# Kernel optimization log

Hardware: AMD Instinct MI355X
Metric: run time of the kernel (lower is better)

The kernel has to match this reference:

```python
import jax, jax.numpy as jnp
import numpy as np

B, T, F, N = 262144, 3, 17, 8
EMBD = 32
DT = 0.2  # 25/5*0.04
EPS = 1e-8  # torch.cosine_similarity eps


def _mono(x, wi, bi, wo, bo):
    # monotonic_fun with increasing=False: relu(-Linear(x)) -> Linear
    h = jax.nn.relu(-(x @ wi.T + bi))  # (..., EMBD)
    return h @ wo.T + bo               # (..., 1)


def _cos(a, b):
    dot = jnp.sum(a * b, axis=-1)
    na = jnp.maximum(jnp.linalg.norm(a, axis=-1), EPS)
    nb = jnp.maximum(jnp.linalg.norm(b, axis=-1), EPS)
    return dot / (na * nb)


def _angle_clamp(vec, e, ang):
    # vec: (B,K,2), e: (B,2) -> keep forces within effective angle cone, sum over K
    keep = jnp.abs(_cos(e[:, None, :], vec)) > ang
    return jnp.sum(vec * keep[..., None], axis=1)


def setup_inputs() -> dict:
    key = jax.random.key(0)
    ks = jax.random.split(key, 8)
    ego = jax.random.normal(ks[0], (B, T, F), jnp.float32)
    ego = ego.at[:, :, 2:4].multiply(10.0)  # position scale
    nei = jax.random.normal(ks[1], (B, N, F), jnp.float32)
    nei = nei.at[:, :, 2:4].multiply(10.0).at[:, :, 4:6].multiply(0.1)
    border = jax.random.normal(ks[2], (4,), jnp.float32)
    attr_dest_para = jax.random.uniform(ks[3], (2,), jnp.float32) + 0.1  # relu(rand), keep away from 0 divisor
    eff_angle = jax.nn.sigmoid(jax.random.uniform(ks[4], (1,), jnp.float32))

    def mlp(k):
        k1, k2, k3, k4 = jax.random.split(k, 4)
        wi = jax.random.uniform(k1, (EMBD, 1), jnp.float32)      # clamped >= 0
        bi = jax.random.normal(k2, (EMBD,), jnp.float32) * 0.1
        wo = jax.random.uniform(k3, (1, EMBD), jnp.float32) * 0.1  # clamped >= 0
        bo = jax.random.normal(k4, (1,), jnp.float32) * 0.1
        return wi, bi, wo, bo

    an = mlp(ks[5])
    rn = mlp(ks[6])
    rb = mlp(ks[7])
    dl = mlp(jax.random.fold_in(key, 99))
    return dict(
        ego=ego, nei=nei, border=border,
        attr_dest_para=attr_dest_para, eff_angle=eff_angle,
        an_wi=an[0], an_bi=an[1], an_wo=an[2], an_bo=an[3],
        rn_wi=rn[0], rn_bi=rn[1], rn_wo=rn[2], rn_bo=rn[3],
        rb_wi=rb[0], rb_bi=rb[1], rb_wo=rb[2], rb_bo=rb[3],
        dl_wi=dl[0], dl_bi=dl[1], dl_wo=dl[2], dl_bo=dl[3],
    )


def reference(ego, nei, border, attr_dest_para, eff_angle,
              an_wi, an_bi, an_wo, an_bo,
              rn_wi, rn_bi, rn_wo, rn_bo,
              rb_wi, rb_bi, rb_wo, rb_bo,
              dl_wi, dl_bi, dl_wo, dl_bo):
    ego_last = ego[:, -1]  # (B,F)

    # --- attr_destination (desired_velocity=None branch) ---
    v34 = ego_last[:, 3:5]
    dv = jnp.stack([jnp.linalg.norm(v34, axis=-1),
                    jnp.zeros(ego.shape[0], ego.dtype)], axis=1)  # (B,2)
    f_dest = ((attr_dest_para[1] * dv - v34) / attr_dest_para[0])[:, None, :]  # (B,1,2)

    # --- attr_repu_neighbors ---
    r = nei[:, :, 2:4] - ego_last[:, None, 2:4]  # (B,N,2)
    mask = nei[:, :, 2:4] == 0                    # (B,N,2)
    r_norm = jnp.linalg.norm(r, axis=-1, keepdims=True)  # (B,N,1)

    # neighbor durality: quirky use of batch element 1, shared across batch
    ids_last = ego[1, -1, 8:-1]  # (8,) neighbor-id columns
    dur = jnp.zeros(N, ego.dtype)
    for t in range(ego.shape[1]):
        dur = dur + jnp.isin(ids_last, ego[1, t, 8:-1]).astype(ego.dtype)

    f_attr = _mono(r_norm, an_wi, an_bi, an_wo, an_bo) * r / r_norm \
             * _mono(dur[:, None], dl_wi, dl_bi, dl_wo, dl_bo)  # (B,N,2)*(N,1)
    f_attr = jnp.where(mask, 0.0, f_attr)

    v_nei = nei[:, :, 4:6]
    b = r_norm \
        + jnp.sum((r + v_nei * DT) ** 2, axis=-1, keepdims=True) \
        - jnp.sum((v_nei * DT) ** 2, axis=-1, keepdims=True)
    b = jnp.sqrt(b) / 2
    f_repu = _mono(b, rn_wi, rn_bi, rn_wo, rn_bo) * r / r_norm
    f_repu = jnp.where(mask, 0.0, f_repu)

    # --- repu_borders (select_lane = [0, -1]) ---
    rb_all = ego_last[:, 3, None] - border        # (B,4)
    rbv = jnp.stack([rb_all[:, 0], rb_all[:, -1]], axis=1)  # (B,2)
    rbn = jnp.abs(rbv)
    f_bor = _mono(rbn[..., None], rb_wi, rb_bi, rb_wo, rb_bo) * (rbv / rbn)[..., None]  # (B,2,1)
    f_bor = jnp.concatenate([jnp.zeros_like(f_bor), f_bor], axis=-1)  # (B,2,2): [0, fy]

    # --- angle clamp + integrate ---
    e = ego_last[:, 4:6]
    e = e / jnp.linalg.norm(e, axis=1, keepdims=True)
    a = (_angle_clamp(f_dest, e, eff_angle)
         + _angle_clamp(f_attr, e, eff_angle) + _angle_clamp(f_repu, e, eff_angle)
         + _angle_clamp(f_bor, e, eff_angle))
    v = ego_last[:, 2:4] + a * DT
    s = ego_last[:, :2] + v * DT
    return jnp.concatenate([s, v, a], axis=1)  # (B,6)
```

## Files before the change

kernel.cpp:

```cpp
#include <hip/hip_runtime.h>

#define DTC 0.2f
#define EPSC 1e-8f


__global__ __launch_bounds__(128) void sfm_pre(
    const float* __restrict__ ego,
    const float* __restrict__ an_wi, const float* __restrict__ an_bi, const float* __restrict__ an_wo,
    const float* __restrict__ rn_wi, const float* __restrict__ rn_bi, const float* __restrict__ rn_wo,
    const float* __restrict__ rb_wi, const float* __restrict__ rb_bi, const float* __restrict__ rb_wo,
    const float* __restrict__ dl_wi, const float* __restrict__ dl_bi,
    const float* __restrict__ dl_wo, const float* __restrict__ dl_bo,
    float* __restrict__ ws)
{
    __shared__ float tk[96], wiwo[96], wobi[96], skn[96], ssw[96], ssb[96];
    int t = threadIdx.x;
    if (t < 96) {
        int f = t >> 5, k = t & 31;
        const float* wip = (f == 0) ? an_wi : ((f == 1) ? rn_wi : rb_wi);
        const float* bip = (f == 0) ? an_bi : ((f == 1) ? rn_bi : rb_bi);
        const float* wop = (f == 0) ? an_wo : ((f == 1) ? rn_wo : rb_wo);
        float wi = wip[k], bi = bip[k], wo = wop[k];
        tk[t]   = -bi / wi;
        wiwo[t] = wi * wo;
        wobi[t] = wo * bi;
    }
    __syncthreads();
    if (t < 96) {
        int f = t >> 5, k = t & 31;
        float my = tk[t];
        int rank = 0;
        for (int m = 0; m < 32; ++m) {
            float o = tk[f * 32 + m];
            rank += (o < my || (o == my && m < k)) ? 1 : 0;
        }
        skn[f * 32 + rank] = my;
        ssw[f * 32 + rank] = wiwo[t];
        ssb[f * 32 + rank] = wobi[t];
    }
    __syncthreads();
    if (t < 96) {
        int f = t >> 5, p = t & 31;
        float sw_ = 0.f, sb_ = 0.f;
        for (int m = p; m < 32; ++m) { sw_ += ssw[f * 32 + m]; sb_ += ssb[f * 32 + m]; }
        int base = 16 + f * 112;
        ws[base + p]      = skn[f * 32 + p];
        ws[base + 32 + p] = sw_;
        ws[base + 65 + p] = sb_;
        if (p == 0) { ws[base + 64] = 0.f; ws[base + 97] = 0.f; }
    }
    if (t >= 96 && t < 104) {
        int j = t - 96;
        const float* base = ego + 51;
        float idv = base[2 * 17 + 8 + j];
        float dur = 0.f;
        for (int tt = 0; tt < 3; ++tt) {
            bool fo = false;
            for (int m = 0; m < 8; ++m) fo = fo || (idv == base[tt * 17 + 8 + m]);
            dur += fo ? 1.f : 0.f;
        }
        float acc = 0.f;
        for (int k = 0; k < 32; ++k)
            acc = fmaf(dl_wo[k], fmaxf(0.f, -fmaf(dl_wi[k], dur, dl_bi[k])), acc);
        ws[j] = acc + dl_bo[0];
    }
}

__device__ __forceinline__ float mono_eval(const float* __restrict__ kn, float x) {
    int i = (kn[15] <= x) ? 16 : 0;
    i += (kn[i + 7] <= x) ? 8 : 0;
    i += (kn[i + 3] <= x) ? 4 : 0;
    i += (kn[i + 1] <= x) ? 2 : 0;
    i += (kn[i] <= x) ? 1 : 0;
    return -fmaf(kn[32 + i], x, kn[65 + i]);
}

__global__ __launch_bounds__(256) void sfm_main(
    const float* __restrict__ ego, const float* __restrict__ nei,
    const float* __restrict__ border, const float* __restrict__ adp,
    const float* __restrict__ eang,
    const float* __restrict__ an_bo, const float* __restrict__ rn_bo,
    const float* __restrict__ rb_bo,
    const float* __restrict__ wsrc,
    float* __restrict__ out, int Bn)
{
    __shared__ float sw[360];
    __shared__ float snei[4352];
    __shared__ float sego[1632];
    __shared__ float sout[192];

    int t = threadIdx.x;
    long long blk = blockIdx.x;

    {
        const float4* nsrc = (const float4*)nei + blk * 1088;
        long long ntot = (long long)Bn * 34;
        float4* nd = (float4*)snei;
#pragma unroll
        for (int i = 0; i < 5; ++i) {
            int idx = t + 256 * i;
            if (idx < 1088 && blk * 1088 + idx < ntot) nd[idx] = nsrc[idx];
        }
        const float4* esrc = (const float4*)ego + blk * 408;
        long long etot = (long long)Bn * 51 / 4;
        float4* ed = (float4*)sego;
#pragma unroll
        for (int i = 0; i < 2; ++i) {
            int idx = t + 256 * i;
            if (idx < 408 && blk * 408 + idx < etot) ed[idx] = esrc[idx];
        }
    }
    for (int i = t; i < 352; i += 256) sw[i] = wsrc[i];
    if (t == 0) sw[352] = an_bo[0];
    if (t == 1) sw[353] = rn_bo[0];
    if (t == 2) sw[354] = rb_bo[0];
    if (t == 3) sw[355] = adp[0];
    if (t == 4) sw[356] = adp[1];
    if (t == 5) sw[357] = eang[0];
    if (t == 6) sw[358] = border[0];
    if (t == 7) sw[359] = border[3];
    __syncthreads();

    int l  = t & 7;
    int r32 = t >> 3;

    const float* eg = sego + 51 * r32 + 34;
    float g0 = eg[0], g1 = eg[1], g2 = eg[2], g3 = eg[3], g4 = eg[4], g5 = eg[5];

    const float* nr = snei + 136 * r32 + 17 * l + 2;
    float nx = nr[0], ny = nr[1], vx = nr[2], vy = nr[3];

    float Rx = nx - g2, Ry = ny - g3;
    float rr = sqrtf(Rx * Rx + Ry * Ry);
    float ax = fmaf(vx, DTC, Rx), ay = fmaf(vy, DTC, Ry);
    float wx = vx * DTC, wy = vy * DTC;
    float bb = sqrtf(rr + ax * ax + ay * ay - wx * wx - wy * wy) * 0.5f;

    float an_bo_v = sw[352], rn_bo_v = sw[353], rb_bo_v = sw[354];
    float p0 = sw[355], p1 = sw[356], ang = sw[357];
    float rb0 = g3 - sw[358], rb1 = g3 - sw[359];
    float rbn0 = fabsf(rb0), rbn1 = fabsf(rb1);

    float fA = mono_eval(sw + 16, rr) + an_bo_v;
    float fR = mono_eval(sw + 128, bb) + rn_bo_v;
    float xb = (l == 1) ? rbn1 : rbn0;
    float vB = 0.f;
    if (l < 2) vB = mono_eval(sw + 240, xb) + rb_bo_v;
    int lb = (t & 63) & ~7;
    float vB0 = __shfl(vB, lb + 0, 64);
    float vB1 = __shfl(vB, lb + 1, 64);

    float elen = sqrtf(g4 * g4 + g5 * g5);
    float ex = g4 / elen, ey = g5 / elen;
    float na = fmaxf(sqrtf(ex * ex + ey * ey), EPSC);

    float axs = 0.f, ays = 0.f;
#define CLAMP_ADD(VX, VY)                                                   \
    {                                                                       \
        float _vx = (VX), _vy = (VY);                                       \
        float _nv = fmaxf(sqrtf(_vx * _vx + _vy * _vy), EPSC);              \
        float _c = (ex * _vx + ey * _vy) / (na * _nv);                      \
        if (fabsf(_c) > ang) { axs += _vx; ays += _vy; }                    \
    }

    float mfx = (nx == 0.f) ? 0.f : 1.f;
    float mfy = (ny == 0.f) ? 0.f : 1.f;

    {
        float coef = fA / rr * sw[l];
        CLAMP_ADD(coef * Rx * mfx, coef * Ry * mfy);
    }
    {
        float coef = fR / rr;
        CLAMP_ADD(coef * Rx * mfx, coef * Ry * mfy);
    }

#pragma unroll
    for (int m = 1; m < 8; m <<= 1) {
        axs += __shfl_xor(axs, m, 64);
        ays += __shfl_xor(ays, m, 64);
    }

    if (l == 0) {
        float dvn = sqrtf(g3 * g3 + g4 * g4);
        CLAMP_ADD((p1 * dvn - g3) / p0, -g4 / p0);
        CLAMP_ADD(0.f, vB0 * (rb0 / rbn0));
        CLAMP_ADD(0.f, vB1 * (rb1 / rbn1));

        float vxo = fmaf(axs, DTC, g2);
        float vyo = fmaf(ays, DTC, g3);
        float* op = sout + 6 * r32;
        op[0] = fmaf(vxo, DTC, g0);
        op[1] = fmaf(vyo, DTC, g1);
        op[2] = vxo; op[3] = vyo;
        op[4] = axs; op[5] = ays;
    }
#undef CLAMP_ADD

    __syncthreads();
    if (t < 192) {
        long long o = blk * 192 + t;
        if (o < (long long)Bn * 6) out[o] = sout[t];
    }
}

extern "C" void kernel_launch(void* const* d_in, const int* in_sizes, int n_in,
                              void* d_out, int out_size, void* d_ws, size_t ws_size,
                              hipStream_t stream) {
    const float* ego    = (const float*)d_in[0];
    const float* nei    = (const float*)d_in[1];
    const float* border = (const float*)d_in[2];
    const float* adp    = (const float*)d_in[3];
    const float* eang   = (const float*)d_in[4];
    const float* an_wi  = (const float*)d_in[5];
    const float* an_bi  = (const float*)d_in[6];
    const float* an_wo  = (const float*)d_in[7];
    const float* an_bo  = (const float*)d_in[8];
    const float* rn_wi  = (const float*)d_in[9];
    const float* rn_bi  = (const float*)d_in[10];
    const float* rn_wo  = (const float*)d_in[11];
    const float* rn_bo  = (const float*)d_in[12];
    const float* rb_wi  = (const float*)d_in[13];
    const float* rb_bi  = (const float*)d_in[14];
    const float* rb_wo  = (const float*)d_in[15];
    const float* rb_bo  = (const float*)d_in[16];
    const float* dl_wi  = (const float*)d_in[17];
    const float* dl_bi  = (const float*)d_in[18];
    const float* dl_wo  = (const float*)d_in[19];
    const float* dl_bo  = (const float*)d_in[20];
    float* out = (float*)d_out;
    float* ws  = (float*)d_ws;

    int Bn = in_sizes[0] / (3 * 17);

    sfm_pre<<<1, 128, 0, stream>>>(ego,
                                   an_wi, an_bi, an_wo,
                                   rn_wi, rn_bi, rn_wo,
                                   rb_wi, rb_bi, rb_wo,
                                   dl_wi, dl_bi, dl_wo, dl_bo, ws);

    int grid = (Bn + 31) / 32;
    sfm_main<<<grid, 256, 0, stream>>>(ego, nei, border, adp, eang,
                                       an_bo, rn_bo, rb_bo,
                                       ws, out, Bn);
}
```

Before: 289.7 us.

## Fuse preprocessing into persistent grid-stride main kernel

Merges the single-block weight-preprocessing kernel into the main kernel, so every block recomputes the sorted knot tables into shared memory and no second launch or workspace round trip is needed. The main kernel becomes persistent: a fixed grid of 1536 blocks loops over 32-row tiles. The output store is also widened to float4. In exchange, each block repeats the small preprocessing work, and each tile iteration now has extra barriers with no overlap between loading and compute.

```diff
diff --git a/kernel.cpp b/kernel.cpp
--- a/kernel.cpp
+++ b/kernel.cpp
@@ -4,50 +4,69 @@
 #define EPSC 1e-8f
 
 
-__global__ __launch_bounds__(128) void sfm_pre(
-    const float* __restrict__ ego,
-    const float* __restrict__ an_wi, const float* __restrict__ an_bi, const float* __restrict__ an_wo,
-    const float* __restrict__ rn_wi, const float* __restrict__ rn_bi, const float* __restrict__ rn_wo,
-    const float* __restrict__ rb_wi, const float* __restrict__ rb_bi, const float* __restrict__ rb_wo,
+__device__ __forceinline__ float mono_eval(const float* __restrict__ kn, float x) {
+    int i = (kn[15] <= x) ? 16 : 0;
+    i += (kn[i + 7] <= x) ? 8 : 0;
+    i += (kn[i + 3] <= x) ? 4 : 0;
+    i += (kn[i + 1] <= x) ? 2 : 0;
+    i += (kn[i] <= x) ? 1 : 0;
+    return -fmaf(kn[32 + i], x, kn[65 + i]);
+}
+
+__global__ __launch_bounds__(256, 6) void sfm_fused(
+    const float* __restrict__ ego, const float* __restrict__ nei,
+    const float* __restrict__ border, const float* __restrict__ adp,
+    const float* __restrict__ eang,
+    const float* __restrict__ an_wi, const float* __restrict__ an_bi,
+    const float* __restrict__ an_wo, const float* __restrict__ an_bo,
+    const float* __restrict__ rn_wi, const float* __restrict__ rn_bi,
+    const float* __restrict__ rn_wo, const float* __restrict__ rn_bo,
+    const float* __restrict__ rb_wi, const float* __restrict__ rb_bi,
+    const float* __restrict__ rb_wo, const float* __restrict__ rb_bo,
     const float* __restrict__ dl_wi, const float* __restrict__ dl_bi,
     const float* __restrict__ dl_wo, const float* __restrict__ dl_bo,
-    float* __restrict__ ws)
+    float* __restrict__ out, int Bn)
 {
-    __shared__ float tk[96], wiwo[96], wobi[96], skn[96], ssw[96], ssb[96];
+    __shared__ __align__(16) float sw[360];
+    __shared__ __align__(16) float snei[4352];
+    __shared__ __align__(16) float sego[1632];
+    __shared__ __align__(16) float sout[192];
+
     int t = threadIdx.x;
+
     if (t < 96) {
         int f = t >> 5, k = t & 31;
         const float* wip = (f == 0) ? an_wi : ((f == 1) ? rn_wi : rb_wi);
         const float* bip = (f == 0) ? an_bi : ((f == 1) ? rn_bi : rb_bi);
         const float* wop = (f == 0) ? an_wo : ((f == 1) ? rn_wo : rb_wo);
         float wi = wip[k], bi = bip[k], wo = wop[k];
-        tk[t]   = -bi / wi;
-        wiwo[t] = wi * wo;
-        wobi[t] = wo * bi;
+        snei[t]       = -bi / wi;
+        snei[96 + t]  = wi * wo;
+        snei[192 + t] = wo * bi;
     }
     __syncthreads();
     if (t < 96) {
         int f = t >> 5, k = t & 31;
-        float my = tk[t];
+        float my = snei[t];
         int rank = 0;
         for (int m = 0; m < 32; ++m) {
-            float o = tk[f * 32 + m];
+            float o = snei[f * 32 + m];
             rank += (o < my || (o == my && m < k)) ? 1 : 0;
         }
-        skn[f * 32 + rank] = my;
-        ssw[f * 32 + rank] = wiwo[t];
-        ssb[f * 32 + rank] = wobi[t];
+        snei[288 + f * 32 + rank] = my;
+        snei[384 + f * 32 + rank] = snei[96 + t];
+        snei[480 + f * 32 + rank] = snei[192 + t];
     }
     __syncthreads();
     if (t < 96) {
         int f = t >> 5, p = t & 31;
         float sw_ = 0.f, sb_ = 0.f;
-        for (int m = p; m < 32; ++m) { sw_ += ssw[f * 32 + m]; sb_ += ssb[f * 32 + m]; }
+        for (int m = p; m < 32; ++m) { sw_ += snei[384 + f * 32 + m]; sb_ += snei[480 + f * 32 + m]; }
         int base = 16 + f * 112;
-        ws[base + p]      = skn[f * 32 + p];
-        ws[base + 32 + p] = sw_;
-        ws[base + 65 + p] = sb_;
-        if (p == 0) { ws[base + 64] = 0.f; ws[base + 97] = 0.f; }
+        sw[base + p]      = snei[288 + f * 32 + p];
+        sw[base + 32 + p] = sw_;
+        sw[base + 65 + p] = sb_;
+        if (p == 0) { sw[base + 64] = 0.f; sw[base + 97] = 0.f; }
     }
     if (t >= 96 && t < 104) {
         int j = t - 96;
@@ -62,145 +81,117 @@
         float acc = 0.f;
         for (int k = 0; k < 32; ++k)
             acc = fmaf(dl_wo[k], fmaxf(0.f, -fmaf(dl_wi[k], dur, dl_bi[k])), acc);
-        ws[j] = acc + dl_bo[0];
-    }
-}
-
-__device__ __forceinline__ float mono_eval(const float* __restrict__ kn, float x) {
-    int i = (kn[15] <= x) ? 16 : 0;
-    i += (kn[i + 7] <= x) ? 8 : 0;
-    i += (kn[i + 3] <= x) ? 4 : 0;
-    i += (kn[i + 1] <= x) ? 2 : 0;
-    i += (kn[i] <= x) ? 1 : 0;
-    return -fmaf(kn[32 + i], x, kn[65 + i]);
-}
-
-__global__ __launch_bounds__(256) void sfm_main(
-    const float* __restrict__ ego, const float* __restrict__ nei,
-    const float* __restrict__ border, const float* __restrict__ adp,
-    const float* __restrict__ eang,
-    const float* __restrict__ an_bo, const float* __restrict__ rn_bo,
-    const float* __restrict__ rb_bo,
-    const float* __restrict__ wsrc,
-    float* __restrict__ out, int Bn)
-{
-    __shared__ float sw[360];
-    __shared__ float snei[4352];
-    __shared__ float sego[1632];
-    __shared__ float sout[192];
-
-    int t = threadIdx.x;
-    long long blk = blockIdx.x;
-
-    {
-        const float4* nsrc = (const float4*)nei + blk * 1088;
-        long long ntot = (long long)Bn * 34;
-        float4* nd = (float4*)snei;
+        sw[j] = acc + dl_bo[0];
+    }
+    if (t == 104) sw[352] = an_bo[0];
+    if (t == 105) sw[353] = rn_bo[0];
+    if (t == 106) sw[354] = rb_bo[0];
+    if (t == 107) sw[355] = adp[0];
+    if (t == 108) sw[356] = adp[1];
+    if (t == 109) sw[357] = eang[0];
+    if (t == 110) sw[358] = border[0];
+    if (t == 111) sw[359] = border[3];
+    __syncthreads();
+
+    int l   = t & 7;
+    int r32 = t >> 3;
+    long long nTiles = ((long long)Bn + 31) >> 5;
+
+    for (long long tt = blockIdx.x; tt < nTiles; tt += gridDim.x) {
+        {
+            const float4* nsrc = (const float4*)nei + tt * 1088;
+            float4* nd = (float4*)snei;
 #pragma unroll
-        for (int i = 0; i < 5; ++i) {
-            int idx = t + 256 * i;
-            if (idx < 1088 && blk * 1088 + idx < ntot) nd[idx] = nsrc[idx];
-        }
-        const float4* esrc = (const float4*)ego + blk * 408;
-        long long etot = (long long)Bn * 51 / 4;
-        float4* ed = (float4*)sego;
+            for (int i = 0; i < 5; ++i) {
+                int idx = t + 256 * i;
+                if (idx < 1088 && tt * 1088 + idx < (long long)Bn * 34) nd[idx] = nsrc[idx];
+            }
+            const float4* esrc = (const float4*)ego + tt * 408;
+            float4* ed = (float4*)sego;
 #pragma unroll
-        for (int i = 0; i < 2; ++i) {
-            int idx = t + 256 * i;
-            if (idx < 408 && blk * 408 + idx < etot) ed[idx] = esrc[idx];
-        }
-    }
-    for (int i = t; i < 352; i += 256) sw[i] = wsrc[i];
-    if (t == 0) sw[352] = an_bo[0];
-    if (t == 1) sw[353] = rn_bo[0];
-    if (t == 2) sw[354] = rb_bo[0];
-    if (t == 3) sw[355] = adp[0];
-    if (t == 4) sw[356] = adp[1];
-    if (t == 5) sw[357] = eang[0];
-    if (t == 6) sw[358] = border[0];
-    if (t == 7) sw[359] = border[3];
-    __syncthreads();
-
-    int l  = t & 7;
-    int r32 = t >> 3;
-
-    const float* eg = sego + 51 * r32 + 34;
-    float g0 = eg[0], g1 = eg[1], g2 = eg[2], g3 = eg[3], g4 = eg[4], g5 = eg[5];
-
-    const float* nr = snei + 136 * r32 + 17 * l + 2;
-    float nx = nr[0], ny = nr[1], vx = nr[2], vy = nr[3];
-
-    float Rx = nx - g2, Ry = ny - g3;
-    float rr = sqrtf(Rx * Rx + Ry * Ry);
-    float ax = fmaf(vx, DTC, Rx), ay = fmaf(vy, DTC, Ry);
-    float wx = vx * DTC, wy = vy * DTC;
-    float bb = sqrtf(rr + ax * ax + ay * ay - wx * wx - wy * wy) * 0.5f;
-
-    float an_bo_v = sw[352], rn_bo_v = sw[353], rb_bo_v = sw[354];
-    float p0 = sw[355], p1 = sw[356], ang = sw[357];
-    float rb0 = g3 - sw[358], rb1 = g3 - sw[359];
-    float rbn0 = fabsf(rb0), rbn1 = fabsf(rb1);
-
-    float fA = mono_eval(sw + 16, rr) + an_bo_v;
-    float fR = mono_eval(sw + 128, bb) + rn_bo_v;
-    float xb = (l == 1) ? rbn1 : rbn0;
-    float vB = 0.f;
-    if (l < 2) vB = mono_eval(sw + 240, xb) + rb_bo_v;
-    int lb = (t & 63) & ~7;
-    float vB0 = __shfl(vB, lb + 0, 64);
-    float vB1 = __shfl(vB, lb + 1, 64);
-
-    float elen = sqrtf(g4 * g4 + g5 * g5);
-    float ex = g4 / elen, ey = g5 / elen;
-    float na = fmaxf(sqrtf(ex * ex + ey * ey), EPSC);
-
-    float axs = 0.f, ays = 0.f;
+            for (int i = 0; i < 2; ++i) {
+                int idx = t + 256 * i;
+                if (idx < 408 && tt * 408 + idx < ((long long)Bn * 51) / 4) ed[idx] = esrc[idx];
+            }
+        }
+        __syncthreads();
+
+        long long row = tt * 32 + r32;
+        if (row < Bn) {
+            const float* eg = sego + 51 * r32 + 34;
+            float g0 = eg[0], g1 = eg[1], g2 = eg[2], g3 = eg[3], g4 = eg[4], g5 = eg[5];
+
+            const float* nr = snei + 136 * r32 + 17 * l + 2;
+            float nx = nr[0], ny = nr[1], vx = nr[2], vy = nr[3];
+
+            float Rx = nx - g2, Ry = ny - g3;
+            float rr = sqrtf(Rx * Rx + Ry * Ry);
+            float ax = fmaf(vx, DTC, Rx), ay = fmaf(vy, DTC, Ry);
+            float wx = vx * DTC, wy = vy * DTC;
+            float bb = sqrtf(rr + ax * ax + ay * ay - wx * wx - wy * wy) * 0.5f;
+
+            float an_bo_v = sw[352], rn_bo_v = sw[353], rb_bo_v = sw[354];
+            float p0 = sw[355], p1 = sw[356], ang = sw[357];
+            float rb0 = g3 - sw[358], rb1 = g3 - sw[359];
+            float rbn0 = fabsf(rb0), rbn1 = fabsf(rb1);
+
+            float fA = mono_eval(sw + 16, rr) + an_bo_v;
+            float fR = mono_eval(sw + 128, bb) + rn_bo_v;
+            float xb = (l == 1) ? rbn1 : rbn0;
+            float vB = 0.f;
+            if (l < 2) vB = mono_eval(sw + 240, xb) + rb_bo_v;
+            int lb = (t & 63) & ~7;
+            float vB0 = __shfl(vB, lb + 0, 64);
+            float vB1 = __shfl(vB, lb + 1, 64);
+
+            float elen = sqrtf(g4 * g4 + g5 * g5);
+            float ex = g4 / elen, ey = g5 / elen;
+            float na = fmaxf(sqrtf(ex * ex + ey * ey), EPSC);
+
+            float axs = 0.f, ays = 0.f;
 #define CLAMP_ADD(VX, VY)                                                   \
-    {                                                                       \
-        float _vx = (VX), _vy = (VY);                                       \
-        float _nv = fmaxf(sqrtf(_vx * _vx + _vy * _vy), EPSC);              \
-        float _c = (ex * _vx + ey * _vy) / (na * _nv);                      \
-        if (fabsf(_c) > ang) { axs += _vx; ays += _vy; }                    \
-    }
-
-    float mfx = (nx == 0.f) ? 0.f : 1.f;
-    float mfy = (ny == 0.f) ? 0.f : 1.f;
-
-    {
-        float coef = fA / rr * sw[l];
-        CLAMP_ADD(coef * Rx * mfx, coef * Ry * mfy);
-    }
-    {
-        float coef = fR / rr;
-        CLAMP_ADD(coef * Rx * mfx, coef * Ry * mfy);
-    }
+            {                                                               \
+                float _vx = (VX), _vy = (VY);                               \
+                float _nv = fmaxf(sqrtf(_vx * _vx + _vy * _vy), EPSC);      \
+                float _c = (ex * _vx + ey * _vy) / (na * _nv);              \
+                if (fabsf(_c) > ang) { axs += _vx; ays += _vy; }            \
+            }
+
+            float mfx = (nx == 0.f) ? 0.f : 1.f;
+            float mfy = (ny == 0.f) ? 0.f : 1.f;
+
+            { float coef = fA / rr * sw[l];  CLAMP_ADD(coef * Rx * mfx, coef * Ry * mfy); }
+            { float coef = fR / rr;          CLAMP_ADD(coef * Rx * mfx, coef * Ry * mfy); }
 
 #pragma unroll
-    for (int m = 1; m < 8; m <<= 1) {
-        axs += __shfl_xor(axs, m, 64);
-        ays += __shfl_xor(ays, m, 64);
-    }
-
-    if (l == 0) {
-        float dvn = sqrtf(g3 * g3 + g4 * g4);
-        CLAMP_ADD((p1 * dvn - g3) / p0, -g4 / p0);
-        CLAMP_ADD(0.f, vB0 * (rb0 / rbn0));
-        CLAMP_ADD(0.f, vB1 * (rb1 / rbn1));
-
-        float vxo = fmaf(axs, DTC, g2);
-        float vyo = fmaf(ays, DTC, g3);
-        float* op = sout + 6 * r32;
-        op[0] = fmaf(vxo, DTC, g0);
-        op[1] = fmaf(vyo, DTC, g1);
-        op[2] = vxo; op[3] = vyo;
-        op[4] = axs; op[5] = ays;
-    }
+            for (int m = 1; m < 8; m <<= 1) {
+                axs += __shfl_xor(axs, m, 64);
+                ays += __shfl_xor(ays, m, 64);
+            }
+
+            if (l == 0) {
+                float dvn = sqrtf(g3 * g3 + g4 * g4);
+                CLAMP_ADD((p1 * dvn - g3) / p0, -g4 / p0);
+                CLAMP_ADD(0.f, vB0 * (rb0 / rbn0));
+                CLAMP_ADD(0.f, vB1 * (rb1 / rbn1));
+
+                float vxo = fmaf(axs, DTC, g2);
+                float vyo = fmaf(ays, DTC, g3);
+                float* op = sout + 6 * r32;
+                op[0] = fmaf(vxo, DTC, g0);
+                op[1] = fmaf(vyo, DTC, g1);
+                op[2] = vxo; op[3] = vyo;
+                op[4] = axs; op[5] = ays;
+            }
 #undef CLAMP_ADD
-
-    __syncthreads();
-    if (t < 192) {
-        long long o = blk * 192 + t;
-        if (o < (long long)Bn * 6) out[o] = sout[t];
+        }
+        __syncthreads();
+
+        if (t < 48) {
+            long long o4 = tt * 48 + t;
+            if (o4 < ((long long)Bn * 6) / 4) ((float4*)out)[o4] = ((const float4*)sout)[t];
+        }
+        __syncthreads();
     }
 }
 
@@ -229,18 +220,14 @@
     const float* dl_wo  = (const float*)d_in[19];
     const float* dl_bo  = (const float*)d_in[20];
     float* out = (float*)d_out;
-    float* ws  = (float*)d_ws;
+    (void)d_ws; (void)ws_size;
 
     int Bn = in_sizes[0] / (3 * 17);
 
-    sfm_pre<<<1, 128, 0, stream>>>(ego,
-                                   an_wi, an_bi, an_wo,
-                                   rn_wi, rn_bi, rn_wo,
-                                   rb_wi, rb_bi, rb_wo,
-                                   dl_wi, dl_bi, dl_wo, dl_bo, ws);
-
-    int grid = (Bn + 31) / 32;
-    sfm_main<<<grid, 256, 0, stream>>>(ego, nei, border, adp, eang,
-                                       an_bo, rn_bo, rb_bo,
-                                       ws, out, Bn);
+    sfm_fused<<<1536, 256, 0, stream>>>(ego, nei, border, adp, eang,
+                                        an_wi, an_bi, an_wo, an_bo,
+                                        rn_wi, rn_bi, rn_wo, rn_bo,
+                                        rb_wi, rb_bi, rb_wo, rb_bo,
+                                        dl_wi, dl_bi, dl_wo, dl_bo,
+                                        out, Bn);
 }
```

Result: no change. 284.1 us (-1.9%).
